# Performance work log

Measured on AMD Instinct MI355X. Metric: run time of the kernel, lower is better.

The kernel has to match this reference:

```python
import jax, jax.numpy as jnp
import numpy as np


def _ln(x, g, b, eps=1e-5):
    m = jnp.mean(x, axis=-1, keepdims=True)
    v = jnp.mean((x - m) ** 2, axis=-1, keepdims=True)
    return (x - m) / jnp.sqrt(v + eps) * g + b


def _win_part(x, ws):
    # (B,H,W,C) -> (B*nW, ws*ws, C)
    B, H, W, C = x.shape
    x = x.reshape(B, H // ws, ws, W // ws, ws, C)
    x = jnp.transpose(x, (0, 1, 3, 2, 4, 5))
    return x.reshape(-1, ws * ws, C)


def _win_rev(w, ws, H, W):
    # (B*nW, ws, ws, C) -> (B,H,W,C)
    C = w.shape[-1]
    B = w.shape[0] // ((H // ws) * (W // ws))
    x = w.reshape(B, H // ws, W // ws, ws, ws, C)
    x = jnp.transpose(x, (0, 1, 3, 2, 4, 5))
    return x.reshape(B, H, W, C)


def _build_mask(H, W, ws, ss):
    # standard Swin SW-MSA mask, built with numpy at trace time (static shapes)
    img = np.zeros((H, W), np.float32)
    cnt = 0
    for hs in (slice(0, -ws), slice(-ws, -ss), slice(-ss, None)):
        for wsl in (slice(0, -ws), slice(-ws, -ss), slice(-ss, None)):
            img[hs, wsl] = cnt
            cnt += 1
    mw = img.reshape(H // ws, ws, W // ws, ws).transpose(0, 2, 1, 3).reshape(-1, ws * ws)
    diff = mw[:, None, :] - mw[:, :, None]  # (nW, N, N)
    return jnp.asarray(np.where(diff != 0, -np.inf, 0.0).astype(np.float32))


def _swin_block(x, H, W, ws, shift, heads, p):
    B, L, C = x.shape
    hd = C // heads
    N = ws * ws
    shortcut = x
    xg = _ln(x, p['ln1_g'], p['ln1_b']).reshape(B, H, W, C)
    mask = None
    if shift > 0:
        xg = jnp.roll(xg, shift=(-shift, -shift), axis=(1, 2))
        mask = _build_mask(H, W, ws, shift)
    xw = _win_part(xg, ws)  # (B_, N, C)
    qkv = xw @ p['qkv_w'] + p['qkv_b']  # (B_, N, 3C)
    qkv = jnp.transpose(qkv.reshape(-1, N, 3, heads, hd), (2, 0, 3, 1, 4))
    q, k, v = qkv[0] * (hd ** -0.5), qkv[1], qkv[2]  # (B_, h, N, hd)
    attn = jnp.einsum('bhnd,bhmd->bhnm', q, k)
    if mask is not None:
        nW = mask.shape[0]
        attn = attn.reshape(B, nW, heads, N, N) + mask[None, :, None]
        attn = attn.reshape(-1, heads, N, N)
    attn = jax.nn.softmax(attn, axis=-1)
    out = jnp.einsum('bhnm,bhmd->bhnd', attn, v)
    out = jnp.transpose(out, (0, 2, 1, 3)).reshape(-1, N, C)
    out = out @ p['proj_w'] + p['proj_b']
    xg = _win_rev(out.reshape(-1, ws, ws, C), ws, H, W)
    if shift > 0:
        xg = jnp.roll(xg, shift=(shift, shift), axis=(1, 2))
    x = shortcut + xg.reshape(B, L, C)
    h = jax.nn.gelu(_ln(x, p['ln2_g'], p['ln2_b']) @ p['fc1_w'] + p['fc1_b'], approximate=False)
    return x + (h @ p['fc2_w'] + p['fc2_b'])


def _patch_merge(x, H, W, g, b, w):
    B, L, C = x.shape
    xg = x.reshape(B, H, W, C)
    xc = jnp.concatenate([xg[:, 0::2, 0::2], xg[:, 1::2, 0::2], xg[:, 0::2, 1::2], xg[:, 1::2, 1::2]], axis=-1)
    xc = xc.reshape(B, (H // 2) * (W // 2), 4 * C)
    return _ln(xc, g, b) @ w


def setup_inputs() -> dict:
    key = jax.random.key(0)
    ks = jax.random.split(key, 16)
    B, H, W, C = 8, 96, 96, 128
    s = 0.02
    d = {'x': jax.random.normal(ks[0], (B, H * W, C), jnp.float32)}
    i = 1
    for pre in ('a_', 'b_'):
        d[pre + 'ln1_g'] = jnp.ones((C,), jnp.float32)
        d[pre + 'ln1_b'] = jnp.zeros((C,), jnp.float32)
        d[pre + 'qkv_w'] = s * jax.random.normal(ks[i], (C, 3 * C), jnp.float32); i += 1
        d[pre + 'qkv_b'] = jnp.zeros((3 * C,), jnp.float32)
        d[pre + 'proj_w'] = s * jax.random.normal(ks[i], (C, C), jnp.float32); i += 1
        d[pre + 'proj_b'] = jnp.zeros((C,), jnp.float32)
        d[pre + 'ln2_g'] = jnp.ones((C,), jnp.float32)
        d[pre + 'ln2_b'] = jnp.zeros((C,), jnp.float32)
        d[pre + 'fc1_w'] = s * jax.random.normal(ks[i], (C, 4 * C), jnp.float32); i += 1
        d[pre + 'fc1_b'] = jnp.zeros((4 * C,), jnp.float32)
        d[pre + 'fc2_w'] = s * jax.random.normal(ks[i], (4 * C, C), jnp.float32); i += 1
        d[pre + 'fc2_b'] = jnp.zeros((C,), jnp.float32)
    d['mln_g'] = jnp.ones((4 * C,), jnp.float32)
    d['mln_b'] = jnp.zeros((4 * C,), jnp.float32)
    d['red_w'] = s * jax.random.normal(ks[i], (4 * C, 2 * C), jnp.float32)
    d['H'] = H
    d['W'] = W
    return d


def reference(x, a_ln1_g, a_ln1_b, a_qkv_w, a_qkv_b, a_proj_w, a_proj_b, a_ln2_g, a_ln2_b, a_fc1_w, a_fc1_b, a_fc2_w, a_fc2_b, b_ln1_g, b_ln1_b, b_qkv_w, b_qkv_b, b_proj_w, b_proj_b, b_ln2_g, b_ln2_b, b_fc1_w, b_fc1_b, b_fc2_w, b_fc2_b, mln_g, mln_b, red_w, H, W):
    heads, ws = 4, 8
    pa = dict(ln1_g=a_ln1_g, ln1_b=a_ln1_b, qkv_w=a_qkv_w, qkv_b=a_qkv_b, proj_w=a_proj_w, proj_b=a_proj_b, ln2_g=a_ln2_g, ln2_b=a_ln2_b, fc1_w=a_fc1_w, fc1_b=a_fc1_b, fc2_w=a_fc2_w, fc2_b=a_fc2_b)
    pb = dict(ln1_g=b_ln1_g, ln1_b=b_ln1_b, qkv_w=b_qkv_w, qkv_b=b_qkv_b, proj_w=b_proj_w, proj_b=b_proj_b, ln2_g=b_ln2_g, ln2_b=b_ln2_b, fc1_w=b_fc1_w, fc1_b=b_fc1_b, fc2_w=b_fc2_w, fc2_b=b_fc2_b)
    x = _swin_block(x, H, W, ws, 0, heads, pa)          # W-MSA
    x = _swin_block(x, H, W, ws, ws // 2, heads, pb)     # SW-MSA
    return _patch_merge(x, H, W, mln_g, mln_b, red_w)    # (B, HW/4, 2C)
```

## Files before the change

kernel.cpp:

```cpp
#include <hip/hip_runtime.h>
#include <hip/hip_bf16.h>

typedef __bf16 bf16_t;
typedef __bf16 bf16x2 __attribute__((ext_vector_type(2)));
typedef __bf16 bf16x8 __attribute__((ext_vector_type(8)));
typedef float floatx4 __attribute__((ext_vector_type(4)));

#define NTOK 73728

__device__ __forceinline__ void gl16(const bf16_t* g, bf16_t* l) {
    __builtin_amdgcn_global_load_lds((const __attribute__((address_space(1))) void*)g,
                                     (__attribute__((address_space(3))) void*)l, 16, 0, 0);
}

struct TPack {
    const float* src[9];
    bf16_t* dst[9];
    int K[9], N[9];
};
__global__ __launch_bounds__(256) void kconv_t9(TPack p) {
    int seg = blockIdx.y;
    int K = p.K[seg], N = p.N[seg];
    int idx = blockIdx.x * 256 + threadIdx.x;
    if (idx >= K * N) return;
    int n = idx / K, k = idx - n * K;
    p.dst[seg][idx] = (bf16_t)p.src[seg][k * N + n];
}

__global__ __launch_bounds__(256) void kln128(const float* __restrict__ x, const float* __restrict__ g,
                                              const float* __restrict__ bta, bf16_t* __restrict__ out, int M) {
    int row = blockIdx.x * 4 + (threadIdx.x >> 6);
    int lane = threadIdx.x & 63;
    if (row >= M) return;
    float2 v = *(const float2*)&x[row * 128 + lane * 2];
    float s = v.x + v.y;
    float sq = v.x * v.x + v.y * v.y;
    #pragma unroll
    for (int d = 1; d < 64; d <<= 1) { s += __shfl_xor(s, d, 64); sq += __shfl_xor(sq, d, 64); }
    float m = s * (1.0f / 128.0f);
    float var = sq * (1.0f / 128.0f) - m * m;
    float inv = 1.0f / sqrtf(var + 1e-5f);
    float2 gg = *(const float2*)&g[lane * 2];
    float2 bb = *(const float2*)&bta[lane * 2];
    bf16x2 o;
    o[0] = (bf16_t)((v.x - m) * inv * gg.x + bb.x);
    o[1] = (bf16_t)((v.y - m) * inv * gg.y + bb.y);
    *(bf16x2*)&out[row * 128 + lane * 2] = o;
}

__global__ __launch_bounds__(256) void kmergeln(const float* __restrict__ x, const float* __restrict__ g,
                                                const float* __restrict__ bta, bf16_t* __restrict__ out) {
    int row = blockIdx.x * 4 + (threadIdx.x >> 6);
    int lane = threadIdx.x & 63;
    int b = row / 2304; int rr = row - b * 2304;
    int i2 = rr / 48, j2 = rr - i2 * 48;
    int q = lane >> 4;
    int cc = (lane & 15) * 8;
    int di = q & 1, dj = q >> 1;
    int src = ((b * 96 + i2 * 2 + di) * 96 + (j2 * 2 + dj)) * 128 + cc;
    float4 a0 = *(const float4*)&x[src];
    float4 a1 = *(const float4*)&x[src + 4];
    float s  = a0.x + a0.y + a0.z + a0.w + a1.x + a1.y + a1.z + a1.w;
    float sq = a0.x*a0.x + a0.y*a0.y + a0.z*a0.z + a0.w*a0.w
             + a1.x*a1.x + a1.y*a1.y + a1.z*a1.z + a1.w*a1.w;
    #pragma unroll
    for (int d = 1; d < 64; d <<= 1) { s += __shfl_xor(s, d, 64); sq += __shfl_xor(sq, d, 64); }
    float m = s * (1.0f / 512.0f);
    float var = sq * (1.0f / 512.0f) - m * m;
    float inv = 1.0f / sqrtf(var + 1e-5f);
    int c = q * 128 + cc;
    float4 g0 = *(const float4*)&g[c];
    float4 g1 = *(const float4*)&g[c + 4];
    float4 b0 = *(const float4*)&bta[c];
    float4 b1 = *(const float4*)&bta[c + 4];
    bf16x8 o;
    o[0] = (bf16_t)((a0.x - m) * inv * g0.x + b0.x);
    o[1] = (bf16_t)((a0.y - m) * inv * g0.y + b0.y);
    o[2] = (bf16_t)((a0.z - m) * inv * g0.z + b0.z);
    o[3] = (bf16_t)((a0.w - m) * inv * g0.w + b0.w);
    o[4] = (bf16_t)((a1.x - m) * inv * g1.x + b1.x);
    o[5] = (bf16_t)((a1.y - m) * inv * g1.y + b1.y);
    o[6] = (bf16_t)((a1.z - m) * inv * g1.z + b1.z);
    o[7] = (bf16_t)((a1.w - m) * inv * g1.w + b1.w);
    *(bf16x8*)&out[row * 512 + c] = o;
}

template<int MODE>
__global__ __launch_bounds__(256, 5) void gemm64x128(const bf16_t* __restrict__ A,
                                                     const bf16_t* __restrict__ Bt,
                                                     const float* __restrict__ bias,
                                                     const float* __restrict__ res,
                                                     float* __restrict__ outf,
                                                     bf16_t* __restrict__ outh,
                                                     int M, int N, int K) {
    alignas(16) __shared__ bf16_t lA[2 * 64 * 32];
    alignas(16) __shared__ bf16_t lB[2 * 128 * 32];
    const int tid = threadIdx.x;
    const int lane = tid & 63;
    const int wv = tid >> 6;
    const int wm = (wv & 1) * 32;
    const int wn = (wv >> 1) * 64;
    const int frow = lane & 15, fq = lane >> 4;
    const int rowA = blockIdx.y * 64;
    const int rowB = blockIdx.x * 128;
    const int sr = tid >> 2, sc = (tid & 3) * 8;
    const bf16_t* pa = A + (size_t)(rowA + sr) * K + sc;
    const bf16_t* pb0 = Bt + (size_t)(rowB + sr) * K + sc;
    const bf16_t* pb1 = Bt + (size_t)(rowB + 64 + sr) * K + sc;
    floatx4 acc[2][4] = {};
    for (int k0 = 0; k0 < K; k0 += 64) {
        __syncthreads();
        gl16(pa  + k0,      &lA[tid * 8]);
        gl16(pa  + k0 + 32, &lA[2048 + tid * 8]);
        gl16(pb0 + k0,      &lB[tid * 8]);
        gl16(pb1 + k0,      &lB[2048 + tid * 8]);
        gl16(pb0 + k0 + 32, &lB[4096 + tid * 8]);
        gl16(pb1 + k0 + 32, &lB[4096 + 2048 + tid * 8]);
        __syncthreads();
        #pragma unroll
        for (int s = 0; s < 2; s++) {
            bf16x8 af[2], bfr[4];
            #pragma unroll
            for (int i = 0; i < 2; i++)
                af[i] = *(const bf16x8*)&lA[s * 2048 + (wm + i * 16 + frow) * 32 + fq * 8];
            #pragma unroll
            for (int j = 0; j < 4; j++)
                bfr[j] = *(const bf16x8*)&lB[s * 4096 + (wn + j * 16 + frow) * 32 + fq * 8];
            #pragma unroll
            for (int i = 0; i < 2; i++)
                #pragma unroll
                for (int j = 0; j < 4; j++)
                    acc[i][j] = __builtin_amdgcn_mfma_f32_16x16x32_bf16(af[i], bfr[j], acc[i][j], 0, 0, 0);
        }
    }
    #pragma unroll
    for (int i = 0; i < 2; i++) {
        #pragma unroll
        for (int j = 0; j < 4; j++) {
            int col = rowB + wn + j * 16 + frow;
            float bs = (MODE == 3) ? 0.0f : bias[col];
            #pragma unroll
            for (int r = 0; r < 4; r++) {
                int row = rowA + wm + i * 16 + fq * 4 + r;
                float v = acc[i][j][r] + bs;
                size_t off = (size_t)row * N + col;
                if (MODE == 0) {
                    outh[off] = (bf16_t)v;
                } else if (MODE == 1) {
                    outf[off] = res[off] + v;
                } else if (MODE == 2) {
                    float u = 1.5957691216057308f * (v + 0.044715f * v * v * v);
                    outh[off] = (bf16_t)(v / (1.0f + __expf(-u)));
                } else {
                    outf[off] = v;
                }
            }
        }
    }
}

__global__ __launch_bounds__(64) void kattn(const bf16_t* __restrict__ qkv, bf16_t* __restrict__ out, int shift) {
    alignas(16) __shared__ bf16_t lp[64 * 64];
    alignas(16) __shared__ bf16_t lv[64 * 32];
    int blk = blockIdx.x;
    int win = blk >> 2, h = blk & 3;
    int b = win / 144; int wr = win - b * 144;
    int wi = wr / 12, wj = wr - wi * 12;
    int ri0 = wi * 8, rj0 = wj * 8;
    int lane = threadIdx.x;
    auto trow = [&](int n) {
        int oi = ri0 + (n >> 3) + shift; oi = (oi >= 96) ? oi - 96 : oi;
        int oj = rj0 + (n & 7) + shift;  oj = (oj >= 96) ? oj - 96 : oj;
        return (b * 96 + oi) * 96 + oj;
    };
    {
        size_t base = (size_t)trow(lane) * 384 + 256 + h * 32;
        *(uint4*)&lv[lane * 32]      = *(const uint4*)&qkv[base];
        *(uint4*)&lv[lane * 32 + 8]  = *(const uint4*)&qkv[base + 8];
        *(uint4*)&lv[lane * 32 + 16] = *(const uint4*)&qkv[base + 16];
        *(uint4*)&lv[lane * 32 + 24] = *(const uint4*)&qkv[base + 24];
    }
    int frow = lane & 15, fk = (lane >> 4) * 8;
    bf16x8 qf[4], kf[4];
    #pragma unroll
    for (int t = 0; t < 4; t++) {
        size_t rq = (size_t)trow(t * 16 + frow) * 384;
        qf[t] = *(const bf16x8*)&qkv[rq + h * 32 + fk];
        kf[t] = *(const bf16x8*)&qkv[rq + 128 + h * 32 + fk];
    }
    floatx4 S[4][4] = {};
    #pragma unroll
    for (int mt = 0; mt < 4; mt++)
        #pragma unroll
        for (int nt = 0; nt < 4; nt++)
            S[mt][nt] = __builtin_amdgcn_mfma_f32_16x16x32_bf16(qf[mt], kf[nt], S[mt][nt], 0, 0, 0);
    const float scale = 0.17677669529663687f;
    #pragma unroll
    for (int mt = 0; mt < 4; mt++)
        #pragma unroll
        for (int nt = 0; nt < 4; nt++)
            #pragma unroll
            for (int r = 0; r < 4; r++) S[mt][nt][r] *= scale;
    if (shift > 0) {
        auto grpn = [&](int n) {
            int ri = ri0 + (n >> 3), rj = rj0 + (n & 7);
            int gr = (ri < 88) ? 0 : ((ri < 92) ? 1 : 2);
            int gc = (rj < 88) ? 0 : ((rj < 92) ? 1 : 2);
            return gr * 3 + gc;
        };
        int gk[4];
        #pragma unroll
        for (int nt = 0; nt < 4; nt++) gk[nt] = grpn(nt * 16 + frow);
        #pragma unroll
        for (int mt = 0; mt < 4; mt++)
            #pragma unroll
            for (int r = 0; r < 4; r++) {
                int gq = grpn(mt * 16 + (lane >> 4) * 4 + r);
                #pragma unroll
                for (int nt = 0; nt < 4; nt++)
                    if (gq != gk[nt]) S[mt][nt][r] = -1e30f;
            }
    }
    #pragma unroll
    for (int mt = 0; mt < 4; mt++) {
        #pragma unroll
        for (int r = 0; r < 4; r++) {
            float mx = fmaxf(fmaxf(S[mt][0][r], S[mt][1][r]), fmaxf(S[mt][2][r], S[mt][3][r]));
            #pragma unroll
            for (int d = 1; d < 16; d <<= 1) mx = fmaxf(mx, __shfl_xor(mx, d, 64));
            float sm = 0.0f;
            #pragma unroll
            for (int nt = 0; nt < 4; nt++) {
                float p = __expf(S[mt][nt][r] - mx);
                S[mt][nt][r] = p;
                sm += p;
            }
            #pragma unroll
            for (int d = 1; d < 16; d <<= 1) sm += __shfl_xor(sm, d, 64);
            float inv = 1.0f / sm;
            #pragma unroll
            for (int nt = 0; nt < 4; nt++) S[mt][nt][r] *= inv;
        }
    }
    #pragma unroll
    for (int mt = 0; mt < 4; mt++)
        #pragma unroll
        for (int nt = 0; nt < 4; nt++)
            #pragma unroll
            for (int r = 0; r < 4; r++)
                lp[(mt * 16 + (lane >> 4) * 4 + r) * 64 + nt * 16 + frow] = (bf16_t)S[mt][nt][r];
    __syncthreads();
    floatx4 O[4][2] = {};
    #pragma unroll
    for (int ks = 0; ks < 2; ks++) {
        bf16x8 vbs[2];
        #pragma unroll
        for (int nt = 0; nt < 2; nt++)
            #pragma unroll
            for (int j = 0; j < 8; j++)
                vbs[nt][j] = lv[(ks * 32 + fk + j) * 32 + nt * 16 + frow];
        #pragma unroll
        for (int mt = 0; mt < 4; mt++) {
            bf16x8 pa = *(const bf16x8*)&lp[(mt * 16 + frow) * 64 + ks * 32 + fk];
            #pragma unroll
            for (int nt = 0; nt < 2; nt++)
                O[mt][nt] = __builtin_amdgcn_mfma_f32_16x16x32_bf16(pa, vbs[nt], O[mt][nt], 0, 0, 0);
        }
    }
    #pragma unroll
    for (int mt = 0; mt < 4; mt++) {
        #pragma unroll
        for (int r = 0; r < 4; r++) {
            int qr = mt * 16 + (lane >> 4) * 4 + r;
            size_t orow = (size_t)trow(qr) * 128 + h * 32;
            #pragma unroll
            for (int nt = 0; nt < 2; nt++)
                out[orow + nt * 16 + frow] = (bf16_t)O[mt][nt][r];
        }
    }
}

extern "C" void kernel_launch(void* const* d_in, const int* in_sizes, int n_in,
                              void* d_out, int out_size, void* d_ws, size_t ws_size,
                              hipStream_t stream) {
    const float* x       = (const float*)d_in[0];
    const float* a_ln1g  = (const float*)d_in[1];
    const float* a_ln1b  = (const float*)d_in[2];
    const float* a_qkvw  = (const float*)d_in[3];
    const float* a_qkvb  = (const float*)d_in[4];
    const float* a_projw = (const float*)d_in[5];
    const float* a_projb = (const float*)d_in[6];
    const float* a_ln2g  = (const float*)d_in[7];
    const float* a_ln2b  = (const float*)d_in[8];
    const float* a_fc1w  = (const float*)d_in[9];
    const float* a_fc1b  = (const float*)d_in[10];
    const float* a_fc2w  = (const float*)d_in[11];
    const float* a_fc2b  = (const float*)d_in[12];
    const float* b_ln1g  = (const float*)d_in[13];
    const float* b_ln1b  = (const float*)d_in[14];
    const float* b_qkvw  = (const float*)d_in[15];
    const float* b_qkvb  = (const float*)d_in[16];
    const float* b_projw = (const float*)d_in[17];
    const float* b_projb = (const float*)d_in[18];
    const float* b_ln2g  = (const float*)d_in[19];
    const float* b_ln2b  = (const float*)d_in[20];
    const float* b_fc1w  = (const float*)d_in[21];
    const float* b_fc1b  = (const float*)d_in[22];
    const float* b_fc2w  = (const float*)d_in[23];
    const float* b_fc2b  = (const float*)d_in[24];
    const float* mlng    = (const float*)d_in[25];
    const float* mlnb    = (const float*)d_in[26];
    const float* redw    = (const float*)d_in[27];
    float* out = (float*)d_out;

    char* p = (char*)d_ws;
    float*  buf_x   = (float*)p;  p += (size_t)NTOK * 128 * 4;
    bf16_t* buf_ln  = (bf16_t*)p; p += (size_t)NTOK * 128 * 2;
    bf16_t* buf_big = (bf16_t*)p; p += (size_t)NTOK * 512 * 2;
    bf16_t* wt      = (bf16_t*)p;
    bf16_t* buf_qkv  = buf_big;
    bf16_t* buf_attn = buf_big + (size_t)NTOK * 384;
    bf16_t* aqkvT  = wt;
    bf16_t* aprojT = aqkvT  + 384 * 128;
    bf16_t* afc1T  = aprojT + 128 * 128;
    bf16_t* afc2T  = afc1T  + 512 * 128;
    bf16_t* bqkvT  = afc2T  + 128 * 512;
    bf16_t* bprojT = bqkvT  + 384 * 128;
    bf16_t* bfc1T  = bprojT + 128 * 128;
    bf16_t* bfc2T  = bfc1T  + 512 * 128;
    bf16_t* redT   = bfc2T  + 128 * 512;

    TPack tp;
    const float* srcs[9] = {a_qkvw, a_projw, a_fc1w, a_fc2w, b_qkvw, b_projw, b_fc1w, b_fc2w, redw};
    bf16_t* dsts[9] = {aqkvT, aprojT, afc1T, afc2T, bqkvT, bprojT, bfc1T, bfc2T, redT};
    int Ks[9] = {128, 128, 128, 512, 128, 128, 128, 512, 512};
    int Ns[9] = {384, 128, 512, 128, 384, 128, 512, 128, 256};
    for (int i = 0; i < 9; i++) { tp.src[i] = srcs[i]; tp.dst[i] = dsts[i]; tp.K[i] = Ks[i]; tp.N[i] = Ns[i]; }
    kconv_t9<<<dim3(512, 9), dim3(256), 0, stream>>>(tp);

    const dim3 blk256(256);
    const int MG = NTOK / 64;

    kln128<<<dim3(NTOK / 4), blk256, 0, stream>>>(x, a_ln1g, a_ln1b, buf_ln, NTOK);
    gemm64x128<0><<<dim3(3, MG), blk256, 0, stream>>>(buf_ln, aqkvT, a_qkvb, nullptr, nullptr, buf_qkv, NTOK, 384, 128);
    kattn<<<dim3(1152 * 4), dim3(64), 0, stream>>>(buf_qkv, buf_attn, 0);
    gemm64x128<1><<<dim3(1, MG), blk256, 0, stream>>>(buf_attn, aprojT, a_projb, x, buf_x, nullptr, NTOK, 128, 128);
    kln128<<<dim3(NTOK / 4), blk256, 0, stream>>>(buf_x, a_ln2g, a_ln2b, buf_ln, NTOK);
    gemm64x128<2><<<dim3(4, MG), blk256, 0, stream>>>(buf_ln, afc1T, a_fc1b, nullptr, nullptr, buf_big, NTOK, 512, 128);
    gemm64x128<1><<<dim3(1, MG), blk256, 0, stream>>>(buf_big, afc2T, a_fc2b, buf_x, buf_x, nullptr, NTOK, 128, 512);

    kln128<<<dim3(NTOK / 4), blk256, 0, stream>>>(buf_x, b_ln1g, b_ln1b, buf_ln, NTOK);
    gemm64x128<0><<<dim3(3, MG), blk256, 0, stream>>>(buf_ln, bqkvT, b_qkvb, nullptr, nullptr, buf_qkv, NTOK, 384, 128);
    kattn<<<dim3(1152 * 4), dim3(64), 0, stream>>>(buf_qkv, buf_attn, 4);
    gemm64x128<1><<<dim3(1, MG), blk256, 0, stream>>>(buf_attn, bprojT, b_projb, buf_x, buf_x, nullptr, NTOK, 128, 128);
    kln128<<<dim3(NTOK / 4), blk256, 0, stream>>>(buf_x, b_ln2g, b_ln2b, buf_ln, NTOK);
    gemm64x128<2><<<dim3(4, MG), blk256, 0, stream>>>(buf_ln, bfc1T, b_fc1b, nullptr, nullptr, buf_big, NTOK, 512, 128);
    gemm64x128<1><<<dim3(1, MG), blk256, 0, stream>>>(buf_big, bfc2T, b_fc2b, buf_x, buf_x, nullptr, NTOK, 128, 512);

    kmergeln<<<dim3(18432 / 4), blk256, 0, stream>>>(buf_x, mlng, mlnb, buf_big);
    gemm64x128<3><<<dim3(2, 288), blk256, 0, stream>>>(buf_big, redT, nullptr, nullptr, out, nullptr, 18432, 256, 512);
}
```

Baseline: 460.6 us.

## Fuse LayerNorm into QKV GEMM and fuse whole MLP into one kernel

Folds LN1 into a new QKV GEMM kernel that normalizes fp32 rows straight into LDS. It also replaces LN2 + fc1(GELU) + fc2(+residual) with a single kernel that keeps the 64x512 hidden activation in LDS, processed in 128-column chunks. This removes the kln128 launches and the round trips of the LN output and the large hidden buffer through global memory. In exchange, the weights are staged synchronously with no double buffering, there are more barriers per block, and the larger LDS footprint lowers occupancy.

```diff
diff --git a/kernel.cpp b/kernel.cpp
--- a/kernel.cpp
+++ b/kernel.cpp
@@ -11,6 +11,54 @@
 __device__ __forceinline__ void gl16(const bf16_t* g, bf16_t* l) {
     __builtin_amdgcn_global_load_lds((const __attribute__((address_space(1))) void*)g,
                                      (__attribute__((address_space(3))) void*)l, 16, 0, 0);
+}
+
+__device__ __forceinline__ void stage128x128(const bf16_t* src, size_t srcStride, bf16_t* lds, int tid) {
+    #pragma unroll
+    for (int i = 0; i < 8; i++) {
+        int c = i * 256 + tid;
+        int p = c >> 9;
+        int row = (c >> 2) & 127;
+        int seg = c & 3;
+        gl16(src + (size_t)row * srcStride + p * 32 + seg * 8, lds + c * 8);
+    }
+}
+
+__device__ __forceinline__ void stage_ln(const float* __restrict__ src, const float* __restrict__ g,
+                                         const float* __restrict__ bta, bf16_t* lnA, int tid) {
+    int r = tid >> 2, q = tid & 3;
+    const float* rowp = src + (size_t)r * 128 + q * 32;
+    float4 v[8];
+    float s = 0.0f, sq = 0.0f;
+    #pragma unroll
+    for (int i = 0; i < 8; i++) {
+        v[i] = *(const float4*)(rowp + i * 4);
+        s += v[i].x + v[i].y + v[i].z + v[i].w;
+        sq += v[i].x * v[i].x + v[i].y * v[i].y + v[i].z * v[i].z + v[i].w * v[i].w;
+    }
+    s += __shfl_xor(s, 1, 64); sq += __shfl_xor(sq, 1, 64);
+    s += __shfl_xor(s, 2, 64); sq += __shfl_xor(sq, 2, 64);
+    float m = s * (1.0f / 128.0f);
+    float inv = rsqrtf(sq * (1.0f / 128.0f) - m * m + 1e-5f);
+    bf16_t* dst = lnA + q * 2048 + r * 32;
+    #pragma unroll
+    for (int i = 0; i < 4; i++) {
+        float4 a = v[2 * i], b = v[2 * i + 1];
+        float4 g0 = *(const float4*)(g + q * 32 + i * 8);
+        float4 g1 = *(const float4*)(g + q * 32 + i * 8 + 4);
+        float4 b0 = *(const float4*)(bta + q * 32 + i * 8);
+        float4 b1 = *(const float4*)(bta + q * 32 + i * 8 + 4);
+        bf16x8 o;
+        o[0] = (bf16_t)((a.x - m) * inv * g0.x + b0.x);
+        o[1] = (bf16_t)((a.y - m) * inv * g0.y + b0.y);
+        o[2] = (bf16_t)((a.z - m) * inv * g0.z + b0.z);
+        o[3] = (bf16_t)((a.w - m) * inv * g0.w + b0.w);
+        o[4] = (bf16_t)((b.x - m) * inv * g1.x + b1.x);
+        o[5] = (bf16_t)((b.y - m) * inv * g1.y + b1.y);
+        o[6] = (bf16_t)((b.z - m) * inv * g1.z + b1.z);
+        o[7] = (bf16_t)((b.w - m) * inv * g1.w + b1.w);
+        *(bf16x8*)(dst + i * 8) = o;
+    }
 }
 
 struct TPack {
@@ -27,62 +75,134 @@
     p.dst[seg][idx] = (bf16_t)p.src[seg][k * N + n];
 }
 
-__global__ __launch_bounds__(256) void kln128(const float* __restrict__ x, const float* __restrict__ g,
-                                              const float* __restrict__ bta, bf16_t* __restrict__ out, int M) {
-    int row = blockIdx.x * 4 + (threadIdx.x >> 6);
-    int lane = threadIdx.x & 63;
-    if (row >= M) return;
-    float2 v = *(const float2*)&x[row * 128 + lane * 2];
-    float s = v.x + v.y;
-    float sq = v.x * v.x + v.y * v.y;
-    #pragma unroll
-    for (int d = 1; d < 64; d <<= 1) { s += __shfl_xor(s, d, 64); sq += __shfl_xor(sq, d, 64); }
-    float m = s * (1.0f / 128.0f);
-    float var = sq * (1.0f / 128.0f) - m * m;
-    float inv = 1.0f / sqrtf(var + 1e-5f);
-    float2 gg = *(const float2*)&g[lane * 2];
-    float2 bb = *(const float2*)&bta[lane * 2];
-    bf16x2 o;
-    o[0] = (bf16_t)((v.x - m) * inv * gg.x + bb.x);
-    o[1] = (bf16_t)((v.y - m) * inv * gg.y + bb.y);
-    *(bf16x2*)&out[row * 128 + lane * 2] = o;
-}
-
-__global__ __launch_bounds__(256) void kmergeln(const float* __restrict__ x, const float* __restrict__ g,
-                                                const float* __restrict__ bta, bf16_t* __restrict__ out) {
-    int row = blockIdx.x * 4 + (threadIdx.x >> 6);
-    int lane = threadIdx.x & 63;
-    int b = row / 2304; int rr = row - b * 2304;
-    int i2 = rr / 48, j2 = rr - i2 * 48;
-    int q = lane >> 4;
-    int cc = (lane & 15) * 8;
-    int di = q & 1, dj = q >> 1;
-    int src = ((b * 96 + i2 * 2 + di) * 96 + (j2 * 2 + dj)) * 128 + cc;
-    float4 a0 = *(const float4*)&x[src];
-    float4 a1 = *(const float4*)&x[src + 4];
-    float s  = a0.x + a0.y + a0.z + a0.w + a1.x + a1.y + a1.z + a1.w;
-    float sq = a0.x*a0.x + a0.y*a0.y + a0.z*a0.z + a0.w*a0.w
-             + a1.x*a1.x + a1.y*a1.y + a1.z*a1.z + a1.w*a1.w;
-    #pragma unroll
-    for (int d = 1; d < 64; d <<= 1) { s += __shfl_xor(s, d, 64); sq += __shfl_xor(sq, d, 64); }
-    float m = s * (1.0f / 512.0f);
-    float var = sq * (1.0f / 512.0f) - m * m;
-    float inv = 1.0f / sqrtf(var + 1e-5f);
-    int c = q * 128 + cc;
-    float4 g0 = *(const float4*)&g[c];
-    float4 g1 = *(const float4*)&g[c + 4];
-    float4 b0 = *(const float4*)&bta[c];
-    float4 b1 = *(const float4*)&bta[c + 4];
-    bf16x8 o;
-    o[0] = (bf16_t)((a0.x - m) * inv * g0.x + b0.x);
-    o[1] = (bf16_t)((a0.y - m) * inv * g0.y + b0.y);
-    o[2] = (bf16_t)((a0.z - m) * inv * g0.z + b0.z);
-    o[3] = (bf16_t)((a0.w - m) * inv * g0.w + b0.w);
-    o[4] = (bf16_t)((a1.x - m) * inv * g1.x + b1.x);
-    o[5] = (bf16_t)((a1.y - m) * inv * g1.y + b1.y);
-    o[6] = (bf16_t)((a1.z - m) * inv * g1.z + b1.z);
-    o[7] = (bf16_t)((a1.w - m) * inv * g1.w + b1.w);
-    *(bf16x8*)&out[row * 512 + c] = o;
+__global__ __launch_bounds__(256, 3) void kqkv(const float* __restrict__ X,
+                                               const float* __restrict__ g, const float* __restrict__ bta,
+                                               const bf16_t* __restrict__ Wt,
+                                               const float* __restrict__ bias,
+                                               bf16_t* __restrict__ out) {
+    alignas(16) __shared__ bf16_t lA[64 * 128];
+    alignas(16) __shared__ bf16_t lB[128 * 128];
+    const int tid = threadIdx.x;
+    const int rowA = blockIdx.y * 64;
+    const int rowB = blockIdx.x * 128;
+    stage_ln(X + (size_t)rowA * 128, g, bta, lA, tid);
+    stage128x128(Wt + (size_t)rowB * 128, 128, lB, tid);
+    __syncthreads();
+    const int lane = tid & 63, wv = tid >> 6;
+    const int wm = (wv & 1) * 32, wn = (wv >> 1) * 64;
+    const int frow = lane & 15, fq = lane >> 4;
+    floatx4 acc[2][4] = {};
+    #pragma unroll
+    for (int kc = 0; kc < 4; kc++) {
+        bf16x8 af[2], bfr[4];
+        #pragma unroll
+        for (int i = 0; i < 2; i++)
+            af[i] = *(const bf16x8*)&lA[kc * 2048 + (wm + i * 16 + frow) * 32 + fq * 8];
+        #pragma unroll
+        for (int j = 0; j < 4; j++)
+            bfr[j] = *(const bf16x8*)&lB[kc * 4096 + (wn + j * 16 + frow) * 32 + fq * 8];
+        #pragma unroll
+        for (int i = 0; i < 2; i++)
+            #pragma unroll
+            for (int j = 0; j < 4; j++)
+                acc[i][j] = __builtin_amdgcn_mfma_f32_16x16x32_bf16(af[i], bfr[j], acc[i][j], 0, 0, 0);
+    }
+    #pragma unroll
+    for (int i = 0; i < 2; i++)
+        #pragma unroll
+        for (int j = 0; j < 4; j++) {
+            int col = rowB + wn + j * 16 + frow;
+            float bs = bias[col];
+            #pragma unroll
+            for (int r = 0; r < 4; r++) {
+                int row = rowA + wm + i * 16 + fq * 4 + r;
+                out[(size_t)row * 384 + col] = (bf16_t)(acc[i][j][r] + bs);
+            }
+        }
+}
+
+__global__ __launch_bounds__(256, 2) void kmlp(float* __restrict__ res,
+                                               const float* __restrict__ g, const float* __restrict__ bta,
+                                               const bf16_t* __restrict__ W1t,
+                                               const float* __restrict__ b1,
+                                               const bf16_t* __restrict__ W2t,
+                                               const float* __restrict__ b2) {
+    alignas(16) __shared__ bf16_t lA[64 * 128];
+    alignas(16) __shared__ bf16_t lW[128 * 128];
+    alignas(16) __shared__ bf16_t lH[64 * 128];
+    const int tid = threadIdx.x;
+    const int rowA = blockIdx.x * 64;
+    const int lane = tid & 63, wv = tid >> 6;
+    const int wm = (wv & 1) * 32, wn = (wv >> 1) * 64;
+    const int frow = lane & 15, fq = lane >> 4;
+    stage_ln(res + (size_t)rowA * 128, g, bta, lA, tid);
+    floatx4 accO[2][4] = {};
+    for (int cn = 0; cn < 4; cn++) {
+        __syncthreads();
+        stage128x128(W1t + (size_t)(cn * 128) * 128, 128, lW, tid);
+        __syncthreads();
+        floatx4 accH[2][4] = {};
+        #pragma unroll
+        for (int kc = 0; kc < 4; kc++) {
+            bf16x8 af[2], bfr[4];
+            #pragma unroll
+            for (int i = 0; i < 2; i++)
+                af[i] = *(const bf16x8*)&lA[kc * 2048 + (wm + i * 16 + frow) * 32 + fq * 8];
+            #pragma unroll
+            for (int j = 0; j < 4; j++)
+                bfr[j] = *(const bf16x8*)&lW[kc * 4096 + (wn + j * 16 + frow) * 32 + fq * 8];
+            #pragma unroll
+            for (int i = 0; i < 2; i++)
+                #pragma unroll
+                for (int j = 0; j < 4; j++)
+                    accH[i][j] = __builtin_amdgcn_mfma_f32_16x16x32_bf16(af[i], bfr[j], accH[i][j], 0, 0, 0);
+        }
+        #pragma unroll
+        for (int j = 0; j < 4; j++) {
+            int col = wn + j * 16 + frow;
+            float bs = b1[cn * 128 + col];
+            #pragma unroll
+            for (int i = 0; i < 2; i++)
+                #pragma unroll
+                for (int r = 0; r < 4; r++) {
+                    int row = wm + i * 16 + fq * 4 + r;
+                    float v = accH[i][j][r] + bs;
+                    float u = 1.5957691216057308f * (v + 0.044715f * v * v * v);
+                    lH[(col >> 5) * 2048 + row * 32 + (col & 31)] = (bf16_t)(v / (1.0f + __expf(-u)));
+                }
+        }
+        __syncthreads();
+        stage128x128(W2t + cn * 128, 512, lW, tid);
+        __syncthreads();
+        #pragma unroll
+        for (int kc = 0; kc < 4; kc++) {
+            bf16x8 af[2], bfr[4];
+            #pragma unroll
+            for (int i = 0; i < 2; i++)
+                af[i] = *(const bf16x8*)&lH[kc * 2048 + (wm + i * 16 + frow) * 32 + fq * 8];
+            #pragma unroll
+            for (int j = 0; j < 4; j++)
+                bfr[j] = *(const bf16x8*)&lW[kc * 4096 + (wn + j * 16 + frow) * 32 + fq * 8];
+            #pragma unroll
+            for (int i = 0; i < 2; i++)
+                #pragma unroll
+                for (int j = 0; j < 4; j++)
+                    accO[i][j] = __builtin_amdgcn_mfma_f32_16x16x32_bf16(af[i], bfr[j], accO[i][j], 0, 0, 0);
+        }
+    }
+    #pragma unroll
+    for (int j = 0; j < 4; j++) {
+        int col = wn + j * 16 + frow;
+        float bs = b2[col];
+        #pragma unroll
+        for (int i = 0; i < 2; i++)
+            #pragma unroll
+            for (int r = 0; r < 4; r++) {
+                int row = rowA + wm + i * 16 + fq * 4 + r;
+                size_t off = (size_t)row * 128 + col;
+                res[off] = res[off] + accO[i][j][r] + bs;
+            }
+    }
 }
 
 template<int MODE>
@@ -144,19 +264,51 @@
                 int row = rowA + wm + i * 16 + fq * 4 + r;
                 float v = acc[i][j][r] + bs;
                 size_t off = (size_t)row * N + col;
-                if (MODE == 0) {
-                    outh[off] = (bf16_t)v;
-                } else if (MODE == 1) {
+                if (MODE == 1) {
                     outf[off] = res[off] + v;
-                } else if (MODE == 2) {
-                    float u = 1.5957691216057308f * (v + 0.044715f * v * v * v);
-                    outh[off] = (bf16_t)(v / (1.0f + __expf(-u)));
                 } else {
                     outf[off] = v;
                 }
             }
         }
     }
+}
+
+__global__ __launch_bounds__(256) void kmergeln(const float* __restrict__ x, const float* __restrict__ g,
+                                                const float* __restrict__ bta, bf16_t* __restrict__ out) {
+    int row = blockIdx.x * 4 + (threadIdx.x >> 6);
+    int lane = threadIdx.x & 63;
+    int b = row / 2304; int rr = row - b * 2304;
+    int i2 = rr / 48, j2 = rr - i2 * 48;
+    int q = lane >> 4;
+    int cc = (lane & 15) * 8;
+    int di = q & 1, dj = q >> 1;
+    int src = ((b * 96 + i2 * 2 + di) * 96 + (j2 * 2 + dj)) * 128 + cc;
+    float4 a0 = *(const float4*)&x[src];
+    float4 a1 = *(const float4*)&x[src + 4];
+    float s  = a0.x + a0.y + a0.z + a0.w + a1.x + a1.y + a1.z + a1.w;
+    float sq = a0.x*a0.x + a0.y*a0.y + a0.z*a0.z + a0.w*a0.w
+             + a1.x*a1.x + a1.y*a1.y + a1.z*a1.z + a1.w*a1.w;
+    #pragma unroll
+    for (int d = 1; d < 64; d <<= 1) { s += __shfl_xor(s, d, 64); sq += __shfl_xor(sq, d, 64); }
+    float m = s * (1.0f / 512.0f);
+    float var = sq * (1.0f / 512.0f) - m * m;
+    float inv = 1.0f / sqrtf(var + 1e-5f);
+    int c = q * 128 + cc;
+    float4 g0 = *(const float4*)&g[c];
+    float4 g1 = *(const float4*)&g[c + 4];
+    float4 b0 = *(const float4*)&bta[c];
+    float4 b1 = *(const float4*)&bta[c + 4];
+    bf16x8 o;
+    o[0] = (bf16_t)((a0.x - m) * inv * g0.x + b0.x);
+    o[1] = (bf16_t)((a0.y - m) * inv * g0.y + b0.y);
+    o[2] = (bf16_t)((a0.z - m) * inv * g0.z + b0.z);
+    o[3] = (bf16_t)((a0.w - m) * inv * g0.w + b0.w);
+    o[4] = (bf16_t)((a1.x - m) * inv * g1.x + b1.x);
+    o[5] = (bf16_t)((a1.y - m) * inv * g1.y + b1.y);
+    o[6] = (bf16_t)((a1.z - m) * inv * g1.z + b1.z);
+    o[7] = (bf16_t)((a1.w - m) * inv * g1.w + b1.w);
+    *(bf16x8*)&out[row * 512 + c] = o;
 }
 
 __global__ __launch_bounds__(64) void kattn(const bf16_t* __restrict__ qkv, bf16_t* __restrict__ out, int shift) {
@@ -315,11 +467,10 @@
 
     char* p = (char*)d_ws;
     float*  buf_x   = (float*)p;  p += (size_t)NTOK * 128 * 4;
-    bf16_t* buf_ln  = (bf16_t*)p; p += (size_t)NTOK * 128 * 2;
-    bf16_t* buf_big = (bf16_t*)p; p += (size_t)NTOK * 512 * 2;
+    bf16_t* buf_qkv = (bf16_t*)p; p += (size_t)NTOK * 384 * 2;
+    bf16_t* buf_attn= (bf16_t*)p; p += (size_t)NTOK * 128 * 2;
+    bf16_t* buf_mrg = (bf16_t*)p; p += (size_t)18432 * 512 * 2;
     bf16_t* wt      = (bf16_t*)p;
-    bf16_t* buf_qkv  = buf_big;
-    bf16_t* buf_attn = buf_big + (size_t)NTOK * 384;
     bf16_t* aqkvT  = wt;
     bf16_t* aprojT = aqkvT  + 384 * 128;
     bf16_t* afc1T  = aprojT + 128 * 128;
@@ -341,22 +492,16 @@
     const dim3 blk256(256);
     const int MG = NTOK / 64;
 
-    kln128<<<dim3(NTOK / 4), blk256, 0, stream>>>(x, a_ln1g, a_ln1b, buf_ln, NTOK);
-    gemm64x128<0><<<dim3(3, MG), blk256, 0, stream>>>(buf_ln, aqkvT, a_qkvb, nullptr, nullptr, buf_qkv, NTOK, 384, 128);
+    kqkv<<<dim3(3, MG), blk256, 0, stream>>>(x, a_ln1g, a_ln1b, aqkvT, a_qkvb, buf_qkv);
     kattn<<<dim3(1152 * 4), dim3(64), 0, stream>>>(buf_qkv, buf_attn, 0);
     gemm64x128<1><<<dim3(1, MG), blk256, 0, stream>>>(buf_attn, aprojT, a_projb, x, buf_x, nullptr, NTOK, 128, 128);
-    kln128<<<dim3(NTOK / 4), blk256, 0, stream>>>(buf_x, a_ln2g, a_ln2b, buf_ln, NTOK);
-    gemm64x128<2><<<dim3(4, MG), blk256, 0, stream>>>(buf_ln, afc1T, a_fc1b, nullptr, nullptr, buf_big, NTOK, 512, 128);
-    gemm64x128<1><<<dim3(1, MG), blk256, 0, stream>>>(buf_big, afc2T, a_fc2b, buf_x, buf_x, nullptr, NTOK, 128, 512);
-
-    kln128<<<dim3(NTOK / 4), blk256, 0, stream>>>(buf_x, b_ln1g, b_ln1b, buf_ln, NTOK);
-    gemm64x128<0><<<dim3(3, MG), blk256, 0, stream>>>(buf_ln, bqkvT, b_qkvb, nullptr, nullptr, buf_qkv, NTOK, 384, 128);
+    kmlp<<<dim3(MG), blk256, 0, stream>>>(buf_x, a_ln2g, a_ln2b, afc1T, a_fc1b, afc2T, a_fc2b);
+
+    kqkv<<<dim3(3, MG), blk256, 0, stream>>>(buf_x, b_ln1g, b_ln1b, bqkvT, b_qkvb, buf_qkv);
     kattn<<<dim3(1152 * 4), dim3(64), 0, stream>>>(buf_qkv, buf_attn, 4);
     gemm64x128<1><<<dim3(1, MG), blk256, 0, stream>>>(buf_attn, bprojT, b_projb, buf_x, buf_x, nullptr, NTOK, 128, 128);
-    kln128<<<dim3(NTOK / 4), blk256, 0, stream>>>(buf_x, b_ln2g, b_ln2b, buf_ln, NTOK);
-    gemm64x128<2><<<dim3(4, MG), blk256, 0, stream>>>(buf_ln, bfc1T, b_fc1b, nullptr, nullptr, buf_big, NTOK, 512, 128);
-    gemm64x128<1><<<dim3(1, MG), blk256, 0, stream>>>(buf_big, bfc2T, b_fc2b, buf_x, buf_x, nullptr, NTOK, 128, 512);
-
-    kmergeln<<<dim3(18432 / 4), blk256, 0, stream>>>(buf_x, mlng, mlnb, buf_big);
-    gemm64x128<3><<<dim3(2, 288), blk256, 0, stream>>>(buf_big, redT, nullptr, nullptr, out, nullptr, 18432, 256, 512);
-}
+    kmlp<<<dim3(MG), blk256, 0, stream>>>(buf_x, b_ln2g, b_ln2b, bfc1T, b_fc1b, bfc2T, b_fc2b);
+
+    kmergeln<<<dim3(18432 / 4), blk256, 0, stream>>>(buf_x, mlng, mlnb, buf_mrg);
+    gemm64x128<3><<<dim3(2, 288), blk256, 0, stream>>>(buf_mrg, redT, nullptr, nullptr, out, nullptr, 18432, 256, 512);
+}
```

Measured after the change: 476.9 us. +3.5%, slower.
